# Optimization experiments

Hardware: AMD Instinct MI355X
Metric: run time of the kernel (lower is better)

## Reference

```python
import jax, jax.numpy as jnp
import numpy as np

NUM_HEADS = 4
SCALE = 0.17677669529663687  # head_dim**-0.5, head_dim=32


def setup_inputs() -> dict:
    key = jax.random.key(0)
    k1, k2 = jax.random.split(key)
    qkv = jax.random.normal(k1, (2048, 144, 384), dtype=jnp.float32)
    mask = jax.random.normal(k2, (1, NUM_HEADS, 144, 144), dtype=jnp.float32)
    return {"qkv": qkv, "mask": mask}


def reference(qkv, mask):
    B, N, C = qkv.shape
    head_dim = C // NUM_HEADS // 3
    # [B,N,3,H,d] -> [3,B,H,N,d]
    qkv = qkv.reshape(B, N, 3, NUM_HEADS, head_dim).transpose(2, 0, 3, 1, 4)
    q, k, v = qkv[0], qkv[1], qkv[2]
    q = q * SCALE
    attn = jnp.einsum('bhnd,bhmd->bhnm', q, k) + mask  # mask broadcasts over B
    attn = jax.nn.softmax(attn, axis=-1)
    out = jnp.einsum('bhnm,bhmd->bhnd', attn, v)  # [B,H,N,d]
    return out.transpose(0, 2, 1, 3).reshape(B, N, C // 3)
```

## Files before the change

### kernel.cpp

```cpp
#include <hip/hip_runtime.h>


using short8 = __attribute__((ext_vector_type(8))) short;
using f32x4  = __attribute__((ext_vector_type(4))) float;

#define SEQ   144
#define NH    4
#define HD    32
#define C3    384
#define OC    128

#define KSTR  56
#define VSTR  168
#define PSTR  168

#define LOG2E 1.4426950408889634f
#define SCALE 0.17677669529663687f

__device__ __forceinline__ unsigned short f2bf(float f) {
  unsigned int u = __float_as_uint(f);
  u += 0x7fffu + ((u >> 16) & 1u);
  return (unsigned short)(u >> 16);
}

__global__ __launch_bounds__(256, 3)
void attn_kernel(const float* __restrict__ qkv,
                 const float* __restrict__ mask,
                 float* __restrict__ out)
{
  __shared__ __align__(16) unsigned short sK [SEQ * KSTR];
  __shared__ __align__(16) unsigned short sVT[HD  * VSTR];
  __shared__ __align__(16) unsigned short sP [4][16 * PSTR];

  const int tid = threadIdx.x;
  const int bid = blockIdx.x;
  const int b = bid >> 2;
  const int h = bid & 3;

  const float* qbase = qkv + (size_t)b * (SEQ * C3) + h * HD;
  const float* kbase = qbase + NH * HD;
  const float* vbase = qbase + 2 * NH * HD;

  {
    const int n0 = tid >> 4;
    const int d2 = (tid & 15) * 2;
    for (int p = 0; p < 9; ++p) {
      int n = p * 16 + n0;
      float2 kv = *(const float2*)(kbase + (size_t)n * C3 + d2);
      unsigned int pk = (unsigned int)f2bf(kv.x) | ((unsigned int)f2bf(kv.y) << 16);
      *(unsigned int*)&sK[n * KSTR + d2] = pk;
    }
  }
  {
    const int d  = tid & 31;
    const int n0 = tid >> 5;
    for (int p = 0; p < 18; ++p) {
      int n = p * 8 + n0;
      float v = vbase[(size_t)n * C3 + d];
      sVT[d * VSTR + n] = f2bf(v);
    }
    const int r  = tid >> 3;
    const int c0 = tid & 7;
    for (int p = 0; p < 3; ++p)
      sVT[r * VSTR + 144 + c0 + p * 8] = 0;
  }
  __syncthreads();

  const int lane = tid & 63;
  const int wv   = tid >> 6;
  const int m    = lane & 15;
  const int quad = lane >> 4;

  unsigned short* pbuf = sP[wv];
  for (int i = 0; i < 4; ++i) {
    int e = lane * 4 + i;
    pbuf[(e >> 4) * PSTR + 144 + (e & 15)] = 0;
  }

  const float qs = SCALE * LOG2E;
  const float* mbase = mask + (size_t)h * SEQ * SEQ;

  for (int s = wv; s < 9; s += 4) {
    short8 afrag;
    {
      const float* qrow = qbase + (size_t)(s * 16 + m) * C3 + quad * 8;
      float4 q0 = *(const float4*)(qrow);
      float4 q1 = *(const float4*)(qrow + 4);
      afrag[0] = (short)f2bf(q0.x * qs); afrag[1] = (short)f2bf(q0.y * qs);
      afrag[2] = (short)f2bf(q0.z * qs); afrag[3] = (short)f2bf(q0.w * qs);
      afrag[4] = (short)f2bf(q1.x * qs); afrag[5] = (short)f2bf(q1.y * qs);
      afrag[6] = (short)f2bf(q1.z * qs); afrag[7] = (short)f2bf(q1.w * qs);
    }

    float S[9][4];
    for (int nt = 0; nt < 9; ++nt) {
      f32x4 c = {0.f, 0.f, 0.f, 0.f};
      short8 bfrag = *(const short8*)&sK[(nt * 16 + m) * KSTR + quad * 8];
      c = __builtin_amdgcn_mfma_f32_16x16x32_bf16(afrag, bfrag, c, 0, 0, 0);
      const float* mrow = mbase + (size_t)(s * 16 + quad * 4) * SEQ + nt * 16 + m;
      S[nt][0] = c[0] + mrow[0 * SEQ] * LOG2E;
      S[nt][1] = c[1] + mrow[1 * SEQ] * LOG2E;
      S[nt][2] = c[2] + mrow[2 * SEQ] * LOG2E;
      S[nt][3] = c[3] + mrow[3 * SEQ] * LOG2E;
    }

    float mx[4], l[4];
    for (int r = 0; r < 4; ++r) {
      float v = S[0][r];
      for (int nt = 1; nt < 9; ++nt) v = fmaxf(v, S[nt][r]);
      v = fmaxf(v, __shfl_xor(v, 1));
      v = fmaxf(v, __shfl_xor(v, 2));
      v = fmaxf(v, __shfl_xor(v, 4));
      v = fmaxf(v, __shfl_xor(v, 8));
      mx[r] = v;
      l[r] = 0.f;
    }
    for (int nt = 0; nt < 9; ++nt)
      for (int r = 0; r < 4; ++r) {
        float p = __builtin_amdgcn_exp2f(S[nt][r] - mx[r]);
        S[nt][r] = p;
        l[r] += p;
      }
    for (int r = 0; r < 4; ++r) {
      float v = l[r];
      v += __shfl_xor(v, 1);
      v += __shfl_xor(v, 2);
      v += __shfl_xor(v, 4);
      v += __shfl_xor(v, 8);
      l[r] = 1.0f / v;
    }

    for (int nt = 0; nt < 9; ++nt)
      for (int r = 0; r < 4; ++r)
        pbuf[(quad * 4 + r) * PSTR + nt * 16 + m] = f2bf(S[nt][r]);

    f32x4 acc0 = {0.f, 0.f, 0.f, 0.f}, acc1 = {0.f, 0.f, 0.f, 0.f};
    for (int kt = 0; kt < 5; ++kt) {
      short8 pa = *(const short8*)&pbuf[m * PSTR + kt * 32 + quad * 8];
      short8 b0 = *(const short8*)&sVT[(m)      * VSTR + kt * 32 + quad * 8];
      short8 b1 = *(const short8*)&sVT[(16 + m) * VSTR + kt * 32 + quad * 8];
      acc0 = __builtin_amdgcn_mfma_f32_16x16x32_bf16(pa, b0, acc0, 0, 0, 0);
      acc1 = __builtin_amdgcn_mfma_f32_16x16x32_bf16(pa, b1, acc1, 0, 0, 0);
    }

    float* orow = out + ((size_t)b * SEQ + s * 16 + quad * 4) * OC + h * HD + m;
    for (int r = 0; r < 4; ++r) {
      orow[r * OC]      = acc0[r] * l[r];
      orow[r * OC + 16] = acc1[r] * l[r];
    }
  }
}

extern "C" void kernel_launch(void* const* d_in, const int* in_sizes, int n_in,
                              void* d_out, int out_size, void* d_ws, size_t ws_size,
                              hipStream_t stream) {
  const float* qkv  = (const float*)d_in[0];
  const float* mask = (const float*)d_in[1];
  float* out = (float*)d_out;
  attn_kernel<<<dim3(2048 * NH), dim3(256), 0, stream>>>(qkv, mask, out);
}
```

Before: 654.7 us.

## Keep softmax probabilities in registers via transposed QK^T and permlane swaps

The score MFMA now computes K·Q^T, so each lane holds one query row and four contiguous key columns. That lets the mask be read with float4 loads and the row max/sum reduced with only two cross-lane shuffles. The per-wave LDS P buffer is removed: probabilities are packed to bf16 with v_cvt_pk_bf16_f32 and rearranged into the PV A-operand layout using permlane32/permlane16 swaps. Dropping the LDS buffer and its writes allows raising launch bounds to 4 blocks per CU, at the cost of more register pressure and reliance on gfx950-specific lane-swap intrinsics.

```diff
diff --git a/kernel.cpp b/kernel.cpp
--- a/kernel.cpp
+++ b/kernel.cpp
@@ -3,6 +3,7 @@
 
 using short8 = __attribute__((ext_vector_type(8))) short;
 using f32x4  = __attribute__((ext_vector_type(4))) float;
+using uint2v = __attribute__((ext_vector_type(2))) unsigned int;
 
 #define SEQ   144
 #define NH    4
@@ -12,7 +13,6 @@
 
 #define KSTR  56
 #define VSTR  168
-#define PSTR  168
 
 #define LOG2E 1.4426950408889634f
 #define SCALE 0.17677669529663687f
@@ -23,14 +23,19 @@
   return (unsigned short)(u >> 16);
 }
 
-__global__ __launch_bounds__(256, 3)
+__device__ __forceinline__ unsigned int cvt_pk_bf16(float lo, float hi) {
+  unsigned int r;
+  asm("v_cvt_pk_bf16_f32 %0, %1, %2" : "=v"(r) : "v"(lo), "v"(hi));
+  return r;
+}
+
+__global__ __launch_bounds__(256, 4)
 void attn_kernel(const float* __restrict__ qkv,
                  const float* __restrict__ mask,
                  float* __restrict__ out)
 {
   __shared__ __align__(16) unsigned short sK [SEQ * KSTR];
   __shared__ __align__(16) unsigned short sVT[HD  * VSTR];
-  __shared__ __align__(16) unsigned short sP [4][16 * PSTR];
 
   const int tid = threadIdx.x;
   const int bid = blockIdx.x;
@@ -44,23 +49,25 @@
   {
     const int n0 = tid >> 4;
     const int d2 = (tid & 15) * 2;
+    #pragma unroll
     for (int p = 0; p < 9; ++p) {
       int n = p * 16 + n0;
-      float2 kv = *(const float2*)(kbase + (size_t)n * C3 + d2);
-      unsigned int pk = (unsigned int)f2bf(kv.x) | ((unsigned int)f2bf(kv.y) << 16);
+      float2 kv2 = *(const float2*)(kbase + (size_t)n * C3 + d2);
+      unsigned int pk = (unsigned int)f2bf(kv2.x) | ((unsigned int)f2bf(kv2.y) << 16);
       *(unsigned int*)&sK[n * KSTR + d2] = pk;
     }
   }
   {
     const int d  = tid & 31;
     const int n0 = tid >> 5;
+    #pragma unroll
     for (int p = 0; p < 18; ++p) {
       int n = p * 8 + n0;
-      float v = vbase[(size_t)n * C3 + d];
-      sVT[d * VSTR + n] = f2bf(v);
+      sVT[d * VSTR + n] = f2bf(vbase[(size_t)n * C3 + d]);
     }
     const int r  = tid >> 3;
     const int c0 = tid & 7;
+    #pragma unroll
     for (int p = 0; p < 3; ++p)
       sVT[r * VSTR + 144 + c0 + p * 8] = 0;
   }
@@ -71,82 +78,89 @@
   const int m    = lane & 15;
   const int quad = lane >> 4;
 
-  unsigned short* pbuf = sP[wv];
-  for (int i = 0; i < 4; ++i) {
-    int e = lane * 4 + i;
-    pbuf[(e >> 4) * PSTR + 144 + (e & 15)] = 0;
-  }
-
   const float qs = SCALE * LOG2E;
   const float* mbase = mask + (size_t)h * SEQ * SEQ;
 
   for (int s = wv; s < 9; s += 4) {
-    short8 afrag;
+    const int qr = s * 16 + m;
+
+    short8 qfrag;
     {
-      const float* qrow = qbase + (size_t)(s * 16 + m) * C3 + quad * 8;
+      const float* qrow = qbase + (size_t)qr * C3 + quad * 8;
       float4 q0 = *(const float4*)(qrow);
       float4 q1 = *(const float4*)(qrow + 4);
-      afrag[0] = (short)f2bf(q0.x * qs); afrag[1] = (short)f2bf(q0.y * qs);
-      afrag[2] = (short)f2bf(q0.z * qs); afrag[3] = (short)f2bf(q0.w * qs);
-      afrag[4] = (short)f2bf(q1.x * qs); afrag[5] = (short)f2bf(q1.y * qs);
-      afrag[6] = (short)f2bf(q1.z * qs); afrag[7] = (short)f2bf(q1.w * qs);
+      qfrag[0] = (short)f2bf(q0.x * qs); qfrag[1] = (short)f2bf(q0.y * qs);
+      qfrag[2] = (short)f2bf(q0.z * qs); qfrag[3] = (short)f2bf(q0.w * qs);
+      qfrag[4] = (short)f2bf(q1.x * qs); qfrag[5] = (short)f2bf(q1.y * qs);
+      qfrag[6] = (short)f2bf(q1.z * qs); qfrag[7] = (short)f2bf(q1.w * qs);
     }
 
-    float S[9][4];
+    float p[9][4];
+    const float* mrow = mbase + (size_t)qr * SEQ + quad * 4;
+    #pragma unroll
     for (int nt = 0; nt < 9; ++nt) {
       f32x4 c = {0.f, 0.f, 0.f, 0.f};
-      short8 bfrag = *(const short8*)&sK[(nt * 16 + m) * KSTR + quad * 8];
-      c = __builtin_amdgcn_mfma_f32_16x16x32_bf16(afrag, bfrag, c, 0, 0, 0);
-      const float* mrow = mbase + (size_t)(s * 16 + quad * 4) * SEQ + nt * 16 + m;
-      S[nt][0] = c[0] + mrow[0 * SEQ] * LOG2E;
-      S[nt][1] = c[1] + mrow[1 * SEQ] * LOG2E;
-      S[nt][2] = c[2] + mrow[2 * SEQ] * LOG2E;
-      S[nt][3] = c[3] + mrow[3 * SEQ] * LOG2E;
+      short8 kfrag = *(const short8*)&sK[(nt * 16 + m) * KSTR + quad * 8];
+      c = __builtin_amdgcn_mfma_f32_16x16x32_bf16(kfrag, qfrag, c, 0, 0, 0);
+      float4 mk = *(const float4*)(mrow + nt * 16);
+      p[nt][0] = c[0] + mk.x * LOG2E;
+      p[nt][1] = c[1] + mk.y * LOG2E;
+      p[nt][2] = c[2] + mk.z * LOG2E;
+      p[nt][3] = c[3] + mk.w * LOG2E;
     }
 
-    float mx[4], l[4];
-    for (int r = 0; r < 4; ++r) {
-      float v = S[0][r];
-      for (int nt = 1; nt < 9; ++nt) v = fmaxf(v, S[nt][r]);
-      v = fmaxf(v, __shfl_xor(v, 1));
-      v = fmaxf(v, __shfl_xor(v, 2));
-      v = fmaxf(v, __shfl_xor(v, 4));
-      v = fmaxf(v, __shfl_xor(v, 8));
-      mx[r] = v;
-      l[r] = 0.f;
+    float t[9];
+    #pragma unroll
+    for (int nt = 0; nt < 9; ++nt)
+      t[nt] = fmaxf(fmaxf(p[nt][0], p[nt][1]), fmaxf(p[nt][2], p[nt][3]));
+    float mx = fmaxf(fmaxf(fmaxf(t[0], t[1]), fmaxf(t[2], t[3])),
+                     fmaxf(fmaxf(t[4], t[5]), fmaxf(t[6], t[7])));
+    mx = fmaxf(mx, t[8]);
+    mx = fmaxf(mx, __shfl_xor(mx, 16));
+    mx = fmaxf(mx, __shfl_xor(mx, 32));
+
+    float s0 = 0.f, s1 = 0.f, s2 = 0.f, s3 = 0.f;
+    #pragma unroll
+    for (int nt = 0; nt < 9; ++nt) {
+      p[nt][0] = __builtin_amdgcn_exp2f(p[nt][0] - mx); s0 += p[nt][0];
+      p[nt][1] = __builtin_amdgcn_exp2f(p[nt][1] - mx); s1 += p[nt][1];
+      p[nt][2] = __builtin_amdgcn_exp2f(p[nt][2] - mx); s2 += p[nt][2];
+      p[nt][3] = __builtin_amdgcn_exp2f(p[nt][3] - mx); s3 += p[nt][3];
     }
-    for (int nt = 0; nt < 9; ++nt)
-      for (int r = 0; r < 4; ++r) {
-        float p = __builtin_amdgcn_exp2f(S[nt][r] - mx[r]);
-        S[nt][r] = p;
-        l[r] += p;
-      }
-    for (int r = 0; r < 4; ++r) {
-      float v = l[r];
-      v += __shfl_xor(v, 1);
-      v += __shfl_xor(v, 2);
-      v += __shfl_xor(v, 4);
-      v += __shfl_xor(v, 8);
-      l[r] = 1.0f / v;
-    }
-
-    for (int nt = 0; nt < 9; ++nt)
-      for (int r = 0; r < 4; ++r)
-        pbuf[(quad * 4 + r) * PSTR + nt * 16 + m] = f2bf(S[nt][r]);
+    float sum = (s0 + s1) + (s2 + s3);
+    sum += __shfl_xor(sum, 16);
+    sum += __shfl_xor(sum, 32);
+    const float il = 1.0f / sum;
 
     f32x4 acc0 = {0.f, 0.f, 0.f, 0.f}, acc1 = {0.f, 0.f, 0.f, 0.f};
+    #pragma unroll
     for (int kt = 0; kt < 5; ++kt) {
-      short8 pa = *(const short8*)&pbuf[m * PSTR + kt * 32 + quad * 8];
-      short8 b0 = *(const short8*)&sVT[(m)      * VSTR + kt * 32 + quad * 8];
-      short8 b1 = *(const short8*)&sVT[(16 + m) * VSTR + kt * 32 + quad * 8];
-      acc0 = __builtin_amdgcn_mfma_f32_16x16x32_bf16(pa, b0, acc0, 0, 0, 0);
-      acc1 = __builtin_amdgcn_mfma_f32_16x16x32_bf16(pa, b1, acc1, 0, 0, 0);
+      unsigned int E0 = cvt_pk_bf16(p[2 * kt][0], p[2 * kt][1]);
+      unsigned int E1 = cvt_pk_bf16(p[2 * kt][2], p[2 * kt][3]);
+      unsigned int O0 = 0, O1 = 0;
+      if (kt < 4) {
+        O0 = cvt_pk_bf16(p[2 * kt + 1][0], p[2 * kt + 1][1]);
+        O1 = cvt_pk_bf16(p[2 * kt + 1][2], p[2 * kt + 1][3]);
+      }
+      uint2v sA  = __builtin_amdgcn_permlane32_swap(E0, O0, false, false);
+      uint2v sB  = __builtin_amdgcn_permlane32_swap(E1, O1, false, false);
+      uint2v w02 = __builtin_amdgcn_permlane16_swap(sA[0], sA[1], false, false);
+      uint2v w13 = __builtin_amdgcn_permlane16_swap(sB[0], sB[1], false, false);
+      union { unsigned int u[4]; short8 v; } pa;
+      pa.u[0] = w02[0]; pa.u[1] = w13[0]; pa.u[2] = w02[1]; pa.u[3] = w13[1];
+
+      short8 b0 = *(const short8*)&sVT[ m        * VSTR + kt * 32 + quad * 8];
+      short8 b1 = *(const short8*)&sVT[(16 + m)  * VSTR + kt * 32 + quad * 8];
+      acc0 = __builtin_amdgcn_mfma_f32_16x16x32_bf16(pa.v, b0, acc0, 0, 0, 0);
+      acc1 = __builtin_amdgcn_mfma_f32_16x16x32_bf16(pa.v, b1, acc1, 0, 0, 0);
     }
 
     float* orow = out + ((size_t)b * SEQ + s * 16 + quad * 4) * OC + h * HD + m;
+    #pragma unroll
     for (int r = 0; r < 4; ++r) {
-      orow[r * OC]      = acc0[r] * l[r];
-      orow[r * OC + 16] = acc1[r] * l[r];
+      float ilr = __shfl(il, quad * 4 + r);
+      orow[r * OC]      = acc0[r] * ilr;
+      orow[r * OC + 16] = acc1[r] * ilr;
     }
   }
 }
```

Result: slower. 668.5 us (+2.1%).
